# Optimization experiments

Hardware: AMD Instinct MI355X
Metric: run time of the kernel (lower is better)

Reference implementation:

```python
import jax, jax.numpy as jnp
import numpy as np

N = 50000
E = 800000
HID = 128
FILT = 128
NG = 50
CUTOFF = 10.0
LOG2 = float(np.log(2.0))


def shifted_softplus(x):
    return jax.nn.softplus(x) - LOG2


def setup_inputs() -> dict:
    key = jax.random.key(0)
    ks = jax.random.split(key, 12)
    s_hid = 1.0 / np.sqrt(HID)
    s_ng = 1.0 / np.sqrt(NG)
    s_f = 1.0 / np.sqrt(FILT)
    return {
        "h": jax.random.normal(ks[0], (N, HID), jnp.float32),
        "pos": jax.random.normal(ks[1], (N, 3), jnp.float32),
        "edge_index": jax.random.randint(ks[2], (2, E), 0, N, jnp.int64),
        # edge filter MLP: Linear(NG->FILT), ssp, Linear(FILT->FILT)
        "mlp_w1": jax.random.uniform(ks[3], (NG, FILT), jnp.float32, -s_ng, s_ng),
        "mlp_b1": jax.random.uniform(ks[4], (FILT,), jnp.float32, -s_ng, s_ng),
        "mlp_w2": jax.random.uniform(ks[5], (FILT, FILT), jnp.float32, -s_f, s_f),
        "mlp_b2": jax.random.uniform(ks[6], (FILT,), jnp.float32, -s_f, s_f),
        # CFConv lin1 (no bias), lin2
        "lin1_w": jax.random.uniform(ks[7], (HID, FILT), jnp.float32, -s_hid, s_hid),
        "lin2_w": jax.random.uniform(ks[8], (FILT, HID), jnp.float32, -s_f, s_f),
        "lin2_b": jax.random.uniform(ks[9], (HID,), jnp.float32, -s_f, s_f),
        # InteractionBlock output linear
        "lin_w": jax.random.uniform(ks[10], (HID, HID), jnp.float32, -s_hid, s_hid),
        "lin_b": jax.random.uniform(ks[11], (HID,), jnp.float32, -s_hid, s_hid),
    }


def reference(h, pos, edge_index, mlp_w1, mlp_b1, mlp_w2, mlp_b2,
              lin1_w, lin2_w, lin2_b, lin_w, lin_b):
    row, col = edge_index[0], edge_index[1]  # target, source (PyG convention)

    # edge distances  [E]
    edge_weight = jnp.linalg.norm(pos[row] - pos[col], axis=-1)

    # GaussianSmearing: offsets linspace(0, cutoff, NG)  -> [E, NG]
    offset = jnp.linspace(0.0, CUTOFF, NG, dtype=h.dtype)
    coeff = -0.5 / (offset[1] - offset[0]) ** 2
    edge_attr = jnp.exp(coeff * (edge_weight[:, None] - offset) ** 2)

    # CFConv: cosine cutoff * filter MLP   -> edge filters W [E, FILT]
    C = 0.5 * (jnp.cos(edge_weight * (jnp.pi / CUTOFF)) + 1.0)
    W = shifted_softplus(edge_attr @ mlp_w1 + mlp_b1) @ mlp_w2 + mlp_b2
    W = W * C[:, None]

    # gather-modulate-scatter message passing
    x = h @ lin1_w                    # [N, FILT]
    msg = x[col] * W                  # [E, FILT]
    agg = jax.ops.segment_sum(msg, row, num_segments=N)  # [N, FILT]
    x = agg @ lin2_w + lin2_b         # [N, HID]

    # InteractionBlock tail
    x = shifted_softplus(x)
    x = x @ lin_w + lin_b
    return x
```

## Files before the change

### kernel.cpp

```cpp
#include <hip/hip_runtime.h>
#include <hip/hip_bf16.h>
#include <math.h>

#define HID   128
#define NG    50
#define TN    8192
#define TMAXD 16.0f
#define RPB   8
#define TSPB  16
#define TBLB  512
#define HB    1024
#define SCAN_CHUNK 1024

typedef __attribute__((ext_vector_type(8))) short bf16x8;
typedef __attribute__((ext_vector_type(4))) float f32x4;
typedef __attribute__((ext_vector_type(4))) int   i32x4;
typedef unsigned short u16;
typedef unsigned int   u32;

#define LOG2F 0.69314718056f

__device__ __forceinline__ float sspf(float v) {
    if (v > 15.f) return v - LOG2F;
    return __logf(1.f + __expf(v)) - LOG2F;
}

__device__ __forceinline__ u16 f2bf(float f) {
    __hip_bfloat16 h = __float2bfloat16(f);
    return *reinterpret_cast<u16*>(&h);
}
__device__ __forceinline__ float bf2f(u32 v) {
    union { u32 u; float f; } x; x.u = v << 16; return x.f;
}

__global__ __launch_bounds__(256) void k1_table_hist_prep(
    const float* __restrict__ w1, const float* __restrict__ b1,
    const float* __restrict__ w2, const float* __restrict__ b2,
    u16* __restrict__ Tn,
    const int* __restrict__ eidx, int* __restrict__ cnt,
    const float* __restrict__ lin1, const float* __restrict__ lin2,
    const float* __restrict__ linw,
    u16* __restrict__ lin1T, u16* __restrict__ lin2T, u16* __restrict__ linwT,
    int E)
{
    __shared__ float sattr[TSPB][64];
    __shared__ float st1[TSPB][128];

    const int tid = threadIdx.x;
    const int b   = blockIdx.x;

    if (b < TBLB) {
        const int s0 = b * TSPB;
        const float TSTEP = TMAXD / TN;
        const float GSTEP = 10.0f / 49.0f;
        const float COEFF = -0.5f / (GSTEP * GSTEP);

        for (int idx = tid; idx < TSPB * 64; idx += 256) {
            int s = idx >> 6, g = idx & 63;
            float v = 0.f;
            if (g < NG) {
                float d = (float)(s0 + s) * TSTEP;
                float t = d - (float)g * GSTEP;
                v = __expf(COEFF * t * t);
            }
            sattr[s][g] = v;
        }
        __syncthreads();

        const int c  = tid & 127;
        const int sh = tid >> 7;

        for (int s = sh; s < TSPB; s += 2) {
            float acc = b1[c];
#pragma unroll
            for (int g = 0; g < NG; ++g)
                acc = fmaf(sattr[s][g], w1[g * 128 + c], acc);
            st1[s][c] = sspf(acc);
        }
        __syncthreads();

        for (int s = sh; s < TSPB; s += 2) {
            float acc = b2[c];
#pragma unroll 8
            for (int k = 0; k < 128; ++k)
                acc = fmaf(st1[s][k], w2[k * 128 + c], acc);
            float d = (float)(s0 + s) * TSTEP;
            float Cf = 0.5f * (__cosf(d * 0.31415926535f) + 1.0f);
            Tn[(size_t)(s0 + s) * HID + c] = f2bf(acc * Cf);
        }
    } else if (b < TBLB + HB) {
        const int hb = b - TBLB;
        for (int e = hb * 256 + tid; e < E; e += HB * 256)
            atomicAdd(&cnt[eidx[e]], 1);
    } else {
        const int wt  = b - TBLB - HB;
        const int wid = wt >> 6;
        const int t   = (wt & 63) * 256 + tid;
        const int n = t >> 7, k = t & 127;
        const float* src = (wid == 0) ? lin1 : (wid == 1) ? lin2 : linw;
        u16* dst = (wid == 0) ? lin1T : (wid == 1) ? lin2T : linwT;
        dst[t] = f2bf(src[k * 128 + n]);
    }
}

__global__ __launch_bounds__(256) void k2_part_mfma(
    const int* __restrict__ cnt, int* __restrict__ part, int nch,
    const float* __restrict__ h, const u16* __restrict__ lin1T,
    u16* __restrict__ bx, int N)
{
    __shared__ u16 sA[64 * 128];
    __shared__ int red[256];
    const int tid = threadIdx.x;

    if ((int)blockIdx.x < nch) {
        const int b = blockIdx.x;
        int base = b * SCAN_CHUNK + tid * 4;
        int s = 0;
#pragma unroll
        for (int i = 0; i < 4; ++i) { int idx = base + i; if (idx < N) s += cnt[idx]; }
        red[tid] = s;
        __syncthreads();
        for (int off = 128; off > 0; off >>= 1) {
            if (tid < off) red[tid] += red[tid + off];
            __syncthreads();
        }
        if (tid == 0) part[b] = red[0];
        return;
    }

    const int r0 = ((int)blockIdx.x - nch) * 64;

    for (int i = tid; i < 64 * 16; i += 256) {
        int row = i >> 4, ck = i & 15;
        i32x4 pk = (i32x4){0, 0, 0, 0};
        if (r0 + row < N) {
            const float* src = h + (size_t)(r0 + row) * HID + ck * 8;
            f32x4 a = *reinterpret_cast<const f32x4*>(src);
            f32x4 c = *reinterpret_cast<const f32x4*>(src + 4);
            pk[0] = (int)((u32)f2bf(a[0]) | ((u32)f2bf(a[1]) << 16));
            pk[1] = (int)((u32)f2bf(a[2]) | ((u32)f2bf(a[3]) << 16));
            pk[2] = (int)((u32)f2bf(c[0]) | ((u32)f2bf(c[1]) << 16));
            pk[3] = (int)((u32)f2bf(c[2]) | ((u32)f2bf(c[3]) << 16));
        }
        int byteoff = row * 256 + ((ck * 16) ^ ((row & 7) << 4));
        *reinterpret_cast<i32x4*>(reinterpret_cast<char*>(sA) + byteoff) = pk;
    }
    __syncthreads();

    const int lane = tid & 63;
    const int wv   = tid >> 6;
    const int l15  = lane & 15;
    const int l4   = lane >> 4;

    bf16x8 bw[2][4];
#pragma unroll
    for (int nt = 0; nt < 2; ++nt)
#pragma unroll
        for (int s = 0; s < 4; ++s) {
            int n = wv * 32 + nt * 16 + l15;
            bw[nt][s] = *reinterpret_cast<const bf16x8*>(lin1T + n * 128 + s * 32 + l4 * 8);
        }

    f32x4 acc[4][2];
#pragma unroll
    for (int mt = 0; mt < 4; ++mt) { acc[mt][0] = (f32x4){0,0,0,0}; acc[mt][1] = (f32x4){0,0,0,0}; }

#pragma unroll
    for (int mt = 0; mt < 4; ++mt)
#pragma unroll
        for (int s = 0; s < 4; ++s) {
            int e = mt * 16 + l15;
            int byteoff = e * 256 + ((s * 64 + l4 * 16) ^ ((e & 7) << 4));
            bf16x8 af = *reinterpret_cast<const bf16x8*>(reinterpret_cast<char*>(sA) + byteoff);
            acc[mt][0] = __builtin_amdgcn_mfma_f32_16x16x32_bf16(af, bw[0][s], acc[mt][0], 0, 0, 0);
            acc[mt][1] = __builtin_amdgcn_mfma_f32_16x16x32_bf16(af, bw[1][s], acc[mt][1], 0, 0, 0);
        }

#pragma unroll
    for (int mt = 0; mt < 4; ++mt)
#pragma unroll
        for (int nt = 0; nt < 2; ++nt)
#pragma unroll
            for (int r = 0; r < 4; ++r) {
                int row = r0 + mt * 16 + l4 * 4 + r;
                if (row < N)
                    bx[(size_t)row * HID + wv * 32 + nt * 16 + l15] = f2bf(acc[mt][nt][r]);
            }
}

__global__ __launch_bounds__(256) void scan_write(
    const int* __restrict__ cnt, const int* __restrict__ part,
    int* __restrict__ cur, int N)
{
    __shared__ int sc[256];
    int b = blockIdx.x, tid = threadIdx.x;
    int base = 0;
    for (int i = 0; i < b; ++i) base += part[i];
    int gbase = b * SCAN_CHUNK + tid * 4;
    int v[4];
#pragma unroll
    for (int i = 0; i < 4; ++i) { int idx = gbase + i; v[i] = (idx < N) ? cnt[idx] : 0; }
    int tsum = v[0] + v[1] + v[2] + v[3];
    sc[tid] = tsum;
    __syncthreads();
    for (int off = 1; off < 256; off <<= 1) {
        int add = (tid >= off) ? sc[tid - off] : 0;
        __syncthreads();
        sc[tid] += add;
        __syncthreads();
    }
    int tpre = base + sc[tid] - tsum;
    int run = 0;
#pragma unroll
    for (int i = 0; i < 4; ++i) {
        int idx = gbase + i;
        if (idx < N) cur[idx] = tpre + run;
        run += v[i];
    }
}

__global__ void scatter2(const int* __restrict__ eidx, const float* __restrict__ pos,
                         int* __restrict__ cur, u32* __restrict__ ec, int E)
{
    for (int e = blockIdx.x * 256 + threadIdx.x; e < E; e += gridDim.x * 256) {
        int r = eidx[e], c = eidx[E + e];
        float dx = pos[3 * r + 0] - pos[3 * c + 0];
        float dy = pos[3 * r + 1] - pos[3 * c + 1];
        float dz = pos[3 * r + 2] - pos[3 * c + 2];
        float d = sqrtf(dx * dx + dy * dy + dz * dz);
        int idx = (int)(d * (TN / TMAXD) + 0.5f);
        idx = min(idx, TN - 1);
        int p = atomicAdd(&cur[r], 1);
        ec[p] = ((u32)idx << 16) | (u32)c;
    }
}

__device__ __forceinline__ void eload4(
    const u32 v[4], const u16* __restrict__ Tn, const u16* __restrict__ bx,
    int c2, u32 T[4], u32 X[4])
{
#pragma unroll
    for (int j = 0; j < 4; ++j) {
        u32 rv = (u32)__builtin_amdgcn_readfirstlane((int)v[j]);
        int is = (int)(rv >> 16);
        int cs = (int)(rv & 0xffffu);
        T[j] = *reinterpret_cast<const u32*>(Tn + (size_t)is * HID + c2);
        X[j] = *reinterpret_cast<const u32*>(bx + (size_t)cs * HID + c2);
    }
}

__device__ __forceinline__ void efma4(
    const u32 T[4], const u32 X[4], float& ax, float& ay)
{
#pragma unroll
    for (int j = 0; j < 4; ++j) {
        ax = fmaf(bf2f(T[j] & 0xffffu), bf2f(X[j] & 0xffffu), ax);
        ay = fmaf(bf2f(T[j] >> 16), bf2f(X[j] >> 16), ay);
    }
}

__device__ __forceinline__ void eone(
    u32 v0, const u16* __restrict__ Tn, const u16* __restrict__ bx,
    int c2, float& ax, float& ay)
{
    u32 rv = (u32)__builtin_amdgcn_readfirstlane((int)v0);
    int is = (int)(rv >> 16);
    int cs = (int)(rv & 0xffffu);
    u32 T0 = *reinterpret_cast<const u32*>(Tn + (size_t)is * HID + c2);
    u32 X0 = *reinterpret_cast<const u32*>(bx + (size_t)cs * HID + c2);
    ax = fmaf(bf2f(T0 & 0xffffu), bf2f(X0 & 0xffffu), ax);
    ay = fmaf(bf2f(T0 >> 16), bf2f(X0 >> 16), ay);
}

__global__ __launch_bounds__(256) void edge_csr(
    const int* __restrict__ rowend,
    const u32* __restrict__ ec,
    const u16* __restrict__ Tn,
    const u16* __restrict__ bx,
    float*     __restrict__ agg,
    int N)
{
    const int lane = threadIdx.x & 63;
    const int slot = threadIdx.x >> 6;
    const int c2   = lane * 2;
    const int r0   = blockIdx.x * RPB;

    const int rA = r0 + slot;
    const int rB = r0 + 4 + slot;

    int eA = 0, eeA = 0, eB = 0, eeB = 0;
    if (rA < N) { eA = (rA == 0) ? 0 : rowend[rA - 1]; eeA = rowend[rA]; }
    if (rB < N) { eB = rowend[rB - 1]; eeB = rowend[rB]; }

    float axA = 0.f, ayA = 0.f, axB = 0.f, ayB = 0.f;
    u32 vA[4], vB[4];
    u32 TA[4], TB[4];
    u32 XA[4], XB[4];

    while (eA + 4 <= eeA && eB + 4 <= eeB) {
#pragma unroll
        for (int j = 0; j < 4; ++j) { vA[j] = ec[eA + j]; vB[j] = ec[eB + j]; }
        eload4(vA, Tn, bx, c2, TA, XA);
        eload4(vB, Tn, bx, c2, TB, XB);
        efma4(TA, XA, axA, ayA);
        efma4(TB, XB, axB, ayB);
        eA += 4; eB += 4;
    }
    while (eA + 4 <= eeA) {
#pragma unroll
        for (int j = 0; j < 4; ++j) vA[j] = ec[eA + j];
        eload4(vA, Tn, bx, c2, TA, XA);
        efma4(TA, XA, axA, ayA);
        eA += 4;
    }
    for (; eA < eeA; ++eA) eone(ec[eA], Tn, bx, c2, axA, ayA);
    while (eB + 4 <= eeB) {
#pragma unroll
        for (int j = 0; j < 4; ++j) vB[j] = ec[eB + j];
        eload4(vB, Tn, bx, c2, TB, XB);
        efma4(TB, XB, axB, ayB);
        eB += 4;
    }
    for (; eB < eeB; ++eB) eone(ec[eB], Tn, bx, c2, axB, ayB);

    if (rA < N) {
        float2 o; o.x = axA; o.y = ayA;
        *reinterpret_cast<float2*>(agg + (size_t)rA * HID + c2) = o;
    }
    if (rB < N) {
        float2 o; o.x = axB; o.y = ayB;
        *reinterpret_cast<float2*>(agg + (size_t)rB * HID + c2) = o;
    }
}

__global__ __launch_bounds__(256) void tail_mfma(
    const float* __restrict__ agg,
    const u16* __restrict__ lin2T, const float* __restrict__ l2b,
    const u16* __restrict__ linwT, const float* __restrict__ linb,
    float* __restrict__ out, int N)
{
    __shared__ u16 sA[64 * 128];
    __shared__ u16 sT[64 * 128];

    const int tid = threadIdx.x;
    const int r0 = blockIdx.x * 64;

    for (int i = tid; i < 64 * 16; i += 256) {
        int row = i >> 4, ck = i & 15;
        i32x4 pk = (i32x4){0, 0, 0, 0};
        if (r0 + row < N) {
            const float* src = agg + (size_t)(r0 + row) * HID + ck * 8;
            f32x4 a = *reinterpret_cast<const f32x4*>(src);
            f32x4 c = *reinterpret_cast<const f32x4*>(src + 4);
            pk[0] = (int)((u32)f2bf(a[0]) | ((u32)f2bf(a[1]) << 16));
            pk[1] = (int)((u32)f2bf(a[2]) | ((u32)f2bf(a[3]) << 16));
            pk[2] = (int)((u32)f2bf(c[0]) | ((u32)f2bf(c[1]) << 16));
            pk[3] = (int)((u32)f2bf(c[2]) | ((u32)f2bf(c[3]) << 16));
        }
        int byteoff = row * 256 + ((ck * 16) ^ ((row & 7) << 4));
        *reinterpret_cast<i32x4*>(reinterpret_cast<char*>(sA) + byteoff) = pk;
    }
    __syncthreads();

    const int lane = tid & 63;
    const int wv   = tid >> 6;
    const int l15  = lane & 15;
    const int l4   = lane >> 4;
    const int n0   = wv * 32 + l15;
    const int n1   = n0 + 16;

    {
        bf16x8 bw[2][4];
#pragma unroll
        for (int nt = 0; nt < 2; ++nt)
#pragma unroll
            for (int s = 0; s < 4; ++s) {
                int n = wv * 32 + nt * 16 + l15;
                bw[nt][s] = *reinterpret_cast<const bf16x8*>(lin2T + n * 128 + s * 32 + l4 * 8);
            }

        f32x4 acc[4][2];
#pragma unroll
        for (int mt = 0; mt < 4; ++mt) { acc[mt][0] = (f32x4){0,0,0,0}; acc[mt][1] = (f32x4){0,0,0,0}; }

#pragma unroll
        for (int mt = 0; mt < 4; ++mt)
#pragma unroll
            for (int s = 0; s < 4; ++s) {
                int e = mt * 16 + l15;
                int byteoff = e * 256 + ((s * 64 + l4 * 16) ^ ((e & 7) << 4));
                bf16x8 af = *reinterpret_cast<const bf16x8*>(reinterpret_cast<char*>(sA) + byteoff);
                acc[mt][0] = __builtin_amdgcn_mfma_f32_16x16x32_bf16(af, bw[0][s], acc[mt][0], 0, 0, 0);
                acc[mt][1] = __builtin_amdgcn_mfma_f32_16x16x32_bf16(af, bw[1][s], acc[mt][1], 0, 0, 0);
            }

        const float bb0 = l2b[n0];
        const float bb1 = l2b[n1];
#pragma unroll
        for (int mt = 0; mt < 4; ++mt)
#pragma unroll
            for (int nt = 0; nt < 2; ++nt) {
                const int n = (nt == 0) ? n0 : n1;
                const float bb = (nt == 0) ? bb0 : bb1;
#pragma unroll
                for (int r = 0; r < 4; ++r) {
                    int m = mt * 16 + l4 * 4 + r;
                    float v = sspf(acc[mt][nt][r] + bb);
                    int byteoff = m * 256 + ((n * 2) ^ ((m & 7) << 4));
                    *reinterpret_cast<u16*>(reinterpret_cast<char*>(sT) + byteoff) = f2bf(v);
                }
            }
    }
    __syncthreads();

    {
        bf16x8 bw[2][4];
#pragma unroll
        for (int nt = 0; nt < 2; ++nt)
#pragma unroll
            for (int s = 0; s < 4; ++s) {
                int n = wv * 32 + nt * 16 + l15;
                bw[nt][s] = *reinterpret_cast<const bf16x8*>(linwT + n * 128 + s * 32 + l4 * 8);
            }

        f32x4 acc[4][2];
#pragma unroll
        for (int mt = 0; mt < 4; ++mt) { acc[mt][0] = (f32x4){0,0,0,0}; acc[mt][1] = (f32x4){0,0,0,0}; }

#pragma unroll
        for (int mt = 0; mt < 4; ++mt)
#pragma unroll
            for (int s = 0; s < 4; ++s) {
                int e = mt * 16 + l15;
                int byteoff = e * 256 + ((s * 64 + l4 * 16) ^ ((e & 7) << 4));
                bf16x8 af = *reinterpret_cast<const bf16x8*>(reinterpret_cast<char*>(sT) + byteoff);
                acc[mt][0] = __builtin_amdgcn_mfma_f32_16x16x32_bf16(af, bw[0][s], acc[mt][0], 0, 0, 0);
                acc[mt][1] = __builtin_amdgcn_mfma_f32_16x16x32_bf16(af, bw[1][s], acc[mt][1], 0, 0, 0);
            }

        const float cb0 = linb[n0];
        const float cb1 = linb[n1];
#pragma unroll
        for (int mt = 0; mt < 4; ++mt)
#pragma unroll
            for (int nt = 0; nt < 2; ++nt) {
                const int n = (nt == 0) ? n0 : n1;
                const float cb = (nt == 0) ? cb0 : cb1;
#pragma unroll
                for (int r = 0; r < 4; ++r) {
                    int row = r0 + mt * 16 + l4 * 4 + r;
                    if (row < N)
                        out[(size_t)row * HID + n] = acc[mt][nt][r] + cb;
                }
            }
    }
}

extern "C" void kernel_launch(void* const* d_in, const int* in_sizes, int n_in,
                              void* d_out, int out_size, void* d_ws, size_t ws_size,
                              hipStream_t stream)
{
    const float* h    = (const float*)d_in[0];
    const float* pos  = (const float*)d_in[1];
    const int*   eidx = (const int*)  d_in[2];
    const float* w1   = (const float*)d_in[3];
    const float* b1   = (const float*)d_in[4];
    const float* w2   = (const float*)d_in[5];
    const float* b2   = (const float*)d_in[6];
    const float* lin1 = (const float*)d_in[7];
    const float* lin2 = (const float*)d_in[8];
    const float* l2b  = (const float*)d_in[9];
    const float* linw = (const float*)d_in[10];
    const float* linb = (const float*)d_in[11];

    const int N = in_sizes[0] / HID;
    const int E = in_sizes[2] / 2;

    char* ws = (char*)d_ws;
    size_t off = 0;
    auto alloc = [&](size_t bytes) { char* p = ws + off; off = (off + bytes + 255) & ~(size_t)255; return p; };

    u16*    bx    = (u16*)   alloc((size_t)N * HID * sizeof(u16));
    u16*    Tn    = (u16*)   alloc((size_t)TN * HID * sizeof(u16));
    float*  agg   = (float*) alloc((size_t)N * HID * sizeof(float));
    int*    cnt   = (int*)   alloc((size_t)N * sizeof(int));
    int*    cur   = (int*)   alloc((size_t)N * sizeof(int));
    int*    part  = (int*)   alloc(256 * sizeof(int));
    u32*    ec    = (u32*)   alloc(((size_t)E + 8) * sizeof(u32));
    u16*    lin1T = (u16*)   alloc(128 * 128 * sizeof(u16));
    u16*    lin2T = (u16*)   alloc(128 * 128 * sizeof(u16));
    u16*    linwT = (u16*)   alloc(128 * 128 * sizeof(u16));

    hipMemsetAsync(cnt, 0, (size_t)N * sizeof(int), stream);

    k1_table_hist_prep<<<TBLB + HB + 192, 256, 0, stream>>>(
        w1, b1, w2, b2, Tn, eidx, cnt, lin1, lin2, linw, lin1T, lin2T, linwT, E);

    const int nch = (N + SCAN_CHUNK - 1) / SCAN_CHUNK;
    const int ngb = (N + 63) / 64;
    k2_part_mfma<<<nch + ngb, 256, 0, stream>>>(cnt, part, nch, h, lin1T, bx, N);

    scan_write<<<nch, 256, 0, stream>>>(cnt, part, cur, N);

    scatter2<<<1024, 256, 0, stream>>>(eidx, pos, cur, ec, E);

    edge_csr<<<(N + RPB - 1) / RPB, 256, 0, stream>>>(cur, ec, Tn, bx, agg, N);

    tail_mfma<<<ngb, 256, 0, stream>>>(agg, lin2T, l2b, linwT, linb, (float*)d_out, N);
}
```

Baseline: 179.8 us.

## Replace global-atomic degree histogram with range-partitioned LDS histogram blocks

The degree count no longer uses 1024 blocks doing global atomicAdd into a zeroed array. Instead, 64 blocks each own a contiguous range of rows, scan every row index with vectorized loads, and count matches with shared-memory atomics. Each block then writes its counts out directly, which also removes the separate memset. The aim is to get rid of contended global atomics and one launch. The cost is that each of the 64 blocks rereads the whole edge-index array, so it uses far fewer blocks and much more total read traffic.

```diff
diff --git a/kernel.cpp b/kernel.cpp
--- a/kernel.cpp
+++ b/kernel.cpp
@@ -9,7 +9,7 @@
 #define RPB   8
 #define TSPB  16
 #define TBLB  512
-#define HB    1024
+#define NHB   64
 #define SCAN_CHUNK 1024
 
 typedef __attribute__((ext_vector_type(8))) short bf16x8;
@@ -41,7 +41,7 @@
     const float* __restrict__ lin1, const float* __restrict__ lin2,
     const float* __restrict__ linw,
     u16* __restrict__ lin1T, u16* __restrict__ lin2T, u16* __restrict__ linwT,
-    int E)
+    int N, int E)
 {
     __shared__ float sattr[TSPB][64];
     __shared__ float st1[TSPB][128];
@@ -88,12 +88,36 @@
             float Cf = 0.5f * (__cosf(d * 0.31415926535f) + 1.0f);
             Tn[(size_t)(s0 + s) * HID + c] = f2bf(acc * Cf);
         }
-    } else if (b < TBLB + HB) {
-        const int hb = b - TBLB;
-        for (int e = hb * 256 + tid; e < E; e += HB * 256)
-            atomicAdd(&cnt[eidx[e]], 1);
+    } else if (b < TBLB + NHB) {
+        int* hcnt = reinterpret_cast<int*>(&sattr[0][0]);
+        const int hb  = b - TBLB;
+        const int rph = (N + NHB - 1) / NHB;
+        const int lo  = hb * rph;
+        const int hi  = min(lo + rph, N);
+        const int nr  = hi - lo;
+
+        for (int i = tid; i < nr; i += 256) hcnt[i] = 0;
+        __syncthreads();
+
+        const int nE4 = E >> 2;
+        const i32x4* p4 = reinterpret_cast<const i32x4*>(eidx);
+        for (int i = tid; i < nE4; i += 256) {
+            i32x4 v = p4[i];
+#pragma unroll
+            for (int j = 0; j < 4; ++j) {
+                int r = v[j];
+                if (r >= lo && r < hi) atomicAdd(&hcnt[r - lo], 1);
+            }
+        }
+        for (int e = (nE4 << 2) + tid; e < E; e += 256) {
+            int r = eidx[e];
+            if (r >= lo && r < hi) atomicAdd(&hcnt[r - lo], 1);
+        }
+        __syncthreads();
+
+        for (int i = tid; i < nr; i += 256) cnt[lo + i] = hcnt[i];
     } else {
-        const int wt  = b - TBLB - HB;
+        const int wt  = b - TBLB - NHB;
         const int wid = wt >> 6;
         const int t   = (wt & 63) * 256 + tid;
         const int n = t >> 7, k = t & 127;
@@ -491,10 +515,8 @@
     u16*    lin2T = (u16*)   alloc(128 * 128 * sizeof(u16));
     u16*    linwT = (u16*)   alloc(128 * 128 * sizeof(u16));
 
-    hipMemsetAsync(cnt, 0, (size_t)N * sizeof(int), stream);
-
-    k1_table_hist_prep<<<TBLB + HB + 192, 256, 0, stream>>>(
-        w1, b1, w2, b2, Tn, eidx, cnt, lin1, lin2, linw, lin1T, lin2T, linwT, E);
+    k1_table_hist_prep<<<TBLB + NHB + 192, 256, 0, stream>>>(
+        w1, b1, w2, b2, Tn, eidx, cnt, lin1, lin2, linw, lin1T, lin2T, linwT, N, E);
 
     const int nch = (N + SCAN_CHUNK - 1) / SCAN_CHUNK;
     const int ngb = (N + 63) / 64;
```

After: 394.1 us. 2.19x slower.
